# Performance work log

Measured on AMD Instinct MI355X. Metric: run time of the kernel, lower is better.

The kernel has to match this reference:

```python
import jax, jax.numpy as jnp
import numpy as np

BLOCK_SIZE = 256


def setup_inputs() -> dict:
    key = jax.random.key(0)
    k1, k2, k3, k4 = jax.random.split(key, 4)
    B, T, C, H = 512, 256, 384, 64
    x = jax.random.normal(k1, (B, T, C), dtype=jnp.float32)
    Wk = jax.random.normal(k2, (H, C), dtype=jnp.float32) * (1.0 / np.sqrt(C))
    Wq = jax.random.normal(k3, (H, C), dtype=jnp.float32) * (1.0 / np.sqrt(C))
    Wv = jax.random.normal(k4, (H, C), dtype=jnp.float32) * (1.0 / np.sqrt(C))
    return {"x": x, "Wk": Wk, "Wq": Wq, "Wv": Wv}


def reference(x, Wk, Wq, Wv):
    # x: [B, T, C]; Wk/Wq/Wv: [H, C] (torch nn.Linear weight layout, bias=False)
    B, T, C = x.shape
    H = Wk.shape[0]
    k = jnp.einsum('btc,hc->bth', x, Wk)
    q = jnp.einsum('btc,hc->bth', x, Wq)
    v = jnp.einsum('btc,hc->bth', x, Wv)
    scale = 1.0 / jnp.sqrt(jnp.float32(H))
    scores = jnp.einsum('bqh,bkh->bqk', q, k) * scale  # [B, T, T]
    causal = jnp.tril(jnp.ones((T, T), dtype=bool))
    scores = jnp.where(causal, scores, -jnp.inf)
    weights = jax.nn.softmax(scores, axis=-1)
    # dropout is identity in eval mode
    out = jnp.einsum('bqk,bkh->bqh', weights, v)  # [B, T, H]
    return out
```

## Files before the change

kernel.cpp:

```cpp
#include <hip/hip_runtime.h>
#include <hip/hip_bf16.h>
#include <math.h>

#define TT 256
#define CC 384
#define HH 64

typedef float v4f   __attribute__((ext_vector_type(4)));
typedef short short8 __attribute__((ext_vector_type(8)));

#define MFMA(a, b, c) __builtin_amdgcn_mfma_f32_16x16x32_bf16((a), (b), (c), 0, 0, 0)

__device__ __forceinline__ unsigned short f2bf(float f) {
    unsigned int u = __float_as_uint(f);
    u += 0x7FFFu + ((u >> 16) & 1u);
    return (unsigned short)(u >> 16);
}

__device__ __forceinline__ ushort4 f2bf4(float4 f) {
    union { __hip_bfloat162 h2[2]; ushort4 u4; } cv;
    cv.h2[0] = __float22bfloat162_rn(make_float2(f.x, f.y));
    cv.h2[1] = __float22bfloat162_rn(make_float2(f.z, f.w));
    return cv.u4;
}

#define KLOOP_BARRIER() do {                                   \
    asm volatile("s_waitcnt lgkmcnt(0)" ::: "memory");         \
    __builtin_amdgcn_s_barrier();                              \
    __builtin_amdgcn_sched_barrier(0);                         \
} while (0)

#define QSCALE 0.18033688f

__global__ __launch_bounds__(512, 4)
void qkv_proj(const float* __restrict__ x, const float* __restrict__ Wkp,
              const float* __restrict__ Wqp, const float* __restrict__ Wvp,
              unsigned short* __restrict__ qg, unsigned short* __restrict__ kg,
              unsigned short* __restrict__ vtg)
{
    __shared__ unsigned short sm[17408];
    unsigned short* x_s = sm;
    unsigned short* w_s = sm + 5120;
    unsigned short* epi = sm;

    const int tid  = threadIdx.x;
    const int wave = tid >> 6;
    const int lane = tid & 63;
    const int col  = lane & 15;
    const int quad = lane >> 4;
    const int row0 = blockIdx.x * 128;

    const int lr  = tid >> 3;
    const int lc4 = (tid & 7) * 4;

    const float* xp  = x   + (size_t)(row0 + lr) * CC + lc4;
    const float* wqp = Wqp + (size_t)lr * CC + lc4;
    const float* wkp = Wkp + (size_t)lr * CC + lc4;
    const float* wvp = Wvp + (size_t)lr * CC + lc4;

    v4f acc[12];
    #pragma unroll
    for (int j = 0; j < 12; ++j) acc[j] = (v4f){0.f, 0.f, 0.f, 0.f};

    float4 xA0 = *(const float4*)(xp);
    float4 xA1 = *(const float4*)(xp + 64 * CC);
    float4 wqA = *(const float4*)(wqp);
    float4 wkA = *(const float4*)(wkp);
    float4 wvA = *(const float4*)(wvp);

    const int afrag_off = (wave * 16 + col) * 40 + quad * 8;

    #pragma unroll
    for (int s = 0; s < 12; ++s) {
        float4 xB0, xB1, wqB, wkB, wvB;
        if (s < 11) {
            const int k0 = (s + 1) * 32;
            xB0 = *(const float4*)(xp + k0);
            xB1 = *(const float4*)(xp + 64 * CC + k0);
            wqB = *(const float4*)(wqp + k0);
            wkB = *(const float4*)(wkp + k0);
            wvB = *(const float4*)(wvp + k0);
        }
        KLOOP_BARRIER();
        *(ushort4*)&x_s[lr * 40 + lc4]         = f2bf4(xA0);
        *(ushort4*)&x_s[(lr + 64) * 40 + lc4]  = f2bf4(xA1);
        *(ushort4*)&w_s[lr * 40 + lc4]         = f2bf4(wqA);
        *(ushort4*)&w_s[(64 + lr) * 40 + lc4]  = f2bf4(wkA);
        *(ushort4*)&w_s[(128 + lr) * 40 + lc4] = f2bf4(wvA);
        KLOOP_BARRIER();
        const short8 a = *(const short8*)&x_s[afrag_off];
        #pragma unroll
        for (int nt = 0; nt < 12; ++nt) {
            const short8 bf = *(const short8*)&w_s[(nt * 16 + col) * 40 + quad * 8];
            acc[nt] = MFMA(a, bf, acc[nt]);
        }
        if (s < 11) { xA0 = xB0; xA1 = xB1; wqA = wqB; wkA = wkB; wvA = wvB; }
    }

    const int b    = row0 >> 8;
    const int half = (row0 >> 7) & 1;

    __syncthreads();
    #pragma unroll
    for (int nt = 0; nt < 8; ++nt) {
        #pragma unroll
        for (int r = 0; r < 4; ++r) {
            const int rl = wave * 16 + quad * 4 + r;
            const int n  = nt * 16 + col;
            float v = acc[nt][r];
            if (nt < 4) v *= QSCALE;
            epi[rl * 136 + n] = f2bf(v);
        }
    }
    __syncthreads();
    #pragma unroll
    for (int p = 0; p < 4; ++p) {
        const int idx = tid + p * 512;
        const int r = idx >> 4, ch = idx & 15;
        const short8 v = *(const short8*)&epi[r * 136 + ch * 8];
        const size_t base = (size_t)(row0 + r) * 64 + (ch & 7) * 8;
        if (ch < 8) *(short8*)&qg[base] = v;
        else        *(short8*)&kg[base] = v;
    }

    __syncthreads();
    #pragma unroll
    for (int nt = 8; nt < 12; ++nt) {
        #pragma unroll
        for (int r = 0; r < 4; ++r) {
            const int rl = wave * 16 + quad * 4 + r;
            const int h  = nt * 16 + col - 128;
            epi[h * 136 + rl] = f2bf(acc[nt][r]);
        }
    }
    __syncthreads();
    #pragma unroll
    for (int p = 0; p < 2; ++p) {
        const int idx = tid + p * 512;
        const int h = idx >> 4, ch = idx & 15;
        const short8 v = *(const short8*)&epi[h * 136 + ch * 8];
        *(short8*)&vtg[((size_t)b * 64 + h) * 256 + half * 128 + ch * 8] = v;
    }
}

__global__ __launch_bounds__(256, 4)
void attn(const unsigned short* __restrict__ qg, const unsigned short* __restrict__ kg,
          const unsigned short* __restrict__ vtg, float* __restrict__ out)
{
    __shared__ unsigned short Pb_all[4 * 16 * 40];
    const int tid  = threadIdx.x;
    const int wave = tid >> 6;
    const int lane = tid & 63;
    const int col  = lane & 15;
    const int quad = lane >> 4;
    const int b    = blockIdx.x >> 1;
    const int g    = blockIdx.x & 1;

    unsigned short* Pb = Pb_all + wave * 640;
    const unsigned short* kb_base = kg  + (size_t)b * 256 * 64;
    const unsigned short* vt_base = vtg + (size_t)b * 64 * 256;

    #pragma unroll
    for (int mi = 0; mi < 2; ++mi) {
        const int j  = g * 4 + wave;
        const int qt = mi ? (15 - j) : j;
        const size_t qoff = ((size_t)b * 256 + qt * 16 + col) * 64 + quad * 8;
        const short8 aq0 = *(const short8*)(qg + qoff);
        const short8 aq1 = *(const short8*)(qg + qoff + 32);

        float lsum[4];
        v4f oacc[4];
        #pragma unroll
        for (int r = 0; r < 4; ++r) lsum[r] = 0.f;
        #pragma unroll
        for (int hn = 0; hn < 4; ++hn) oacc[hn] = (v4f){0.f, 0.f, 0.f, 0.f};

        const int nch = qt / 2 + 1;
        short8 b00, b01, b10, b11;
        {
            const int ko0 = col * 64 + quad * 8;
            const int ko1 = (16 + col) * 64 + quad * 8;
            b00 = *(const short8*)(kb_base + ko0);
            b01 = *(const short8*)(kb_base + ko0 + 32);
            b10 = *(const short8*)(kb_base + ko1);
            b11 = *(const short8*)(kb_base + ko1 + 32);
        }
        for (int kc = 0; kc < nch; ++kc) {
            const int kb = kc * 32;
            v4f s0 = (v4f){0.f, 0.f, 0.f, 0.f};
            v4f s1 = (v4f){0.f, 0.f, 0.f, 0.f};
            s0 = MFMA(aq0, b00, s0);
            s0 = MFMA(aq1, b01, s0);
            s1 = MFMA(aq0, b10, s1);
            s1 = MFMA(aq1, b11, s1);
            if (kc + 1 < nch) {
                const int ko0 = (kb + 32 + col) * 64 + quad * 8;
                const int ko1 = (kb + 48 + col) * 64 + quad * 8;
                b00 = *(const short8*)(kb_base + ko0);
                b01 = *(const short8*)(kb_base + ko0 + 32);
                b10 = *(const short8*)(kb_base + ko1);
                b11 = *(const short8*)(kb_base + ko1 + 32);
            }
            const bool diag = (kc == qt / 2);
            #pragma unroll
            for (int r = 0; r < 4; ++r) {
                const int t = qt * 16 + quad * 4 + r;
                float v0 = s0[r];
                float v1 = s1[r];
                if (diag) {
                    if (kb + col > t)      v0 = -1e30f;
                    if (kb + 16 + col > t) v1 = -1e30f;
                }
                const float p0 = exp2f(v0);
                const float p1 = exp2f(v1);
                lsum[r] += p0 + p1;
                Pb[(quad * 4 + r) * 40 + col]      = f2bf(p0);
                Pb[(quad * 4 + r) * 40 + 16 + col] = f2bf(p1);
            }
            __threadfence_block();
            const short8 ap = *(const short8*)&Pb[col * 40 + quad * 8];
            #pragma unroll
            for (int hn = 0; hn < 4; ++hn) {
                const short8 bv = *(const short8*)(vt_base + (hn * 16 + col) * 256 + kb + quad * 8);
                oacc[hn] = MFMA(ap, bv, oacc[hn]);
            }
        }

        #pragma unroll
        for (int r = 0; r < 4; ++r) {
            float l = lsum[r];
            l += __shfl_xor(l, 1);
            l += __shfl_xor(l, 2);
            l += __shfl_xor(l, 4);
            l += __shfl_xor(l, 8);
            const int t = qt * 16 + quad * 4 + r;
            const float inv = 1.0f / l;
            float* op = out + ((size_t)b * TT + t) * HH;
            #pragma unroll
            for (int hn = 0; hn < 4; ++hn)
                op[hn * 16 + col] = oacc[hn][r] * inv;
        }
    }
}

extern "C" void kernel_launch(void* const* d_in, const int* in_sizes, int n_in,
                              void* d_out, int out_size, void* d_ws, size_t ws_size,
                              hipStream_t stream) {
    const float* x  = (const float*)d_in[0];
    const float* Wk = (const float*)d_in[1];
    const float* Wq = (const float*)d_in[2];
    const float* Wv = (const float*)d_in[3];
    float* out = (float*)d_out;

    unsigned short* qg  = (unsigned short*)d_ws;
    unsigned short* kg  = qg + (size_t)512 * 256 * 64;
    unsigned short* vtg = kg + (size_t)512 * 256 * 64;

    qkv_proj<<<dim3(1024), dim3(512), 0, stream>>>(x, Wk, Wq, Wv, qg, kg, vtg);
    attn<<<dim3(1024), dim3(256), 0, stream>>>(qg, kg, vtg, out);
}
```

Before: 334.6 us.

## Fuse QKV projection and causal attention into one kernel with LDS-resident Q/K/V

Replaces the two-kernel pipeline with a single kernel, one block per batch. The block projects all 256 rows of Q, K and V into LDS in MFMA-fragment-friendly layouts, then runs causal attention straight from LDS. This removes writing Q/K/V^T to a global workspace and reading them back, plus one kernel launch. In exchange it needs about 124KB of LDS per block, which limits residency to one block per CU and cuts the number of blocks in flight.

```diff
diff --git a/kernel.cpp b/kernel.cpp
--- a/kernel.cpp
+++ b/kernel.cpp
@@ -32,141 +32,112 @@
 
 #define QSCALE 0.18033688f
 
-__global__ __launch_bounds__(512, 4)
-void qkv_proj(const float* __restrict__ x, const float* __restrict__ Wkp,
-              const float* __restrict__ Wqp, const float* __restrict__ Wvp,
-              unsigned short* __restrict__ qg, unsigned short* __restrict__ kg,
-              unsigned short* __restrict__ vtg)
+#define XS_OFF 0
+#define WS_OFF 5120
+#define QF_OFF 12800
+#define KF_OFF 29184
+#define VF_OFF 45568
+#define SM_TOTAL 61952
+
+__global__ __launch_bounds__(512, 2)
+void fused_attn(const float* __restrict__ x, const float* __restrict__ Wkp,
+                const float* __restrict__ Wqp, const float* __restrict__ Wvp,
+                float* __restrict__ out)
 {
-    __shared__ unsigned short sm[17408];
-    unsigned short* x_s = sm;
-    unsigned short* w_s = sm + 5120;
-    unsigned short* epi = sm;
+    __shared__ unsigned short sm[SM_TOTAL];
+    unsigned short* x_s = sm + XS_OFF;
+    unsigned short* w_s = sm + WS_OFF;
 
     const int tid  = threadIdx.x;
     const int wave = tid >> 6;
     const int lane = tid & 63;
     const int col  = lane & 15;
     const int quad = lane >> 4;
-    const int row0 = blockIdx.x * 128;
+    const int b    = blockIdx.x;
 
     const int lr  = tid >> 3;
     const int lc4 = (tid & 7) * 4;
 
-    const float* xp  = x   + (size_t)(row0 + lr) * CC + lc4;
     const float* wqp = Wqp + (size_t)lr * CC + lc4;
     const float* wkp = Wkp + (size_t)lr * CC + lc4;
     const float* wvp = Wvp + (size_t)lr * CC + lc4;
 
-    v4f acc[12];
-    #pragma unroll
-    for (int j = 0; j < 12; ++j) acc[j] = (v4f){0.f, 0.f, 0.f, 0.f};
-
-    float4 xA0 = *(const float4*)(xp);
-    float4 xA1 = *(const float4*)(xp + 64 * CC);
-    float4 wqA = *(const float4*)(wqp);
-    float4 wkA = *(const float4*)(wkp);
-    float4 wvA = *(const float4*)(wvp);
-
     const int afrag_off = (wave * 16 + col) * 40 + quad * 8;
 
-    #pragma unroll
-    for (int s = 0; s < 12; ++s) {
-        float4 xB0, xB1, wqB, wkB, wvB;
-        if (s < 11) {
-            const int k0 = (s + 1) * 32;
-            xB0 = *(const float4*)(xp + k0);
-            xB1 = *(const float4*)(xp + 64 * CC + k0);
-            wqB = *(const float4*)(wqp + k0);
-            wkB = *(const float4*)(wkp + k0);
-            wvB = *(const float4*)(wvp + k0);
-        }
-        KLOOP_BARRIER();
-        *(ushort4*)&x_s[lr * 40 + lc4]         = f2bf4(xA0);
-        *(ushort4*)&x_s[(lr + 64) * 40 + lc4]  = f2bf4(xA1);
-        *(ushort4*)&w_s[lr * 40 + lc4]         = f2bf4(wqA);
-        *(ushort4*)&w_s[(64 + lr) * 40 + lc4]  = f2bf4(wkA);
-        *(ushort4*)&w_s[(128 + lr) * 40 + lc4] = f2bf4(wvA);
-        KLOOP_BARRIER();
-        const short8 a = *(const short8*)&x_s[afrag_off];
+    #pragma unroll 1
+    for (int half = 0; half < 2; ++half) {
+        const float* xp = x + ((size_t)b * 256 + half * 128 + lr) * CC + lc4;
+
+        v4f acc[12];
+        #pragma unroll
+        for (int j = 0; j < 12; ++j) acc[j] = (v4f){0.f, 0.f, 0.f, 0.f};
+
+        float4 xA0 = *(const float4*)(xp);
+        float4 xA1 = *(const float4*)(xp + 64 * CC);
+        float4 wqA = *(const float4*)(wqp);
+        float4 wkA = *(const float4*)(wkp);
+        float4 wvA = *(const float4*)(wvp);
+
+        #pragma unroll
+        for (int s = 0; s < 12; ++s) {
+            float4 xB0, xB1, wqB, wkB, wvB;
+            if (s < 11) {
+                const int k0 = (s + 1) * 32;
+                xB0 = *(const float4*)(xp + k0);
+                xB1 = *(const float4*)(xp + 64 * CC + k0);
+                wqB = *(const float4*)(wqp + k0);
+                wkB = *(const float4*)(wkp + k0);
+                wvB = *(const float4*)(wvp + k0);
+            }
+            KLOOP_BARRIER();
+            *(ushort4*)&x_s[lr * 40 + lc4]         = f2bf4(xA0);
+            *(ushort4*)&x_s[(lr + 64) * 40 + lc4]  = f2bf4(xA1);
+            *(ushort4*)&w_s[lr * 40 + lc4]         = f2bf4(wqA);
+            *(ushort4*)&w_s[(64 + lr) * 40 + lc4]  = f2bf4(wkA);
+            *(ushort4*)&w_s[(128 + lr) * 40 + lc4] = f2bf4(wvA);
+            KLOOP_BARRIER();
+            const short8 a = *(const short8*)&x_s[afrag_off];
+            #pragma unroll
+            for (int nt = 0; nt < 12; ++nt) {
+                const short8 bf = *(const short8*)&w_s[(nt * 16 + col) * 40 + quad * 8];
+                acc[nt] = MFMA(a, bf, acc[nt]);
+            }
+            if (s < 11) { xA0 = xB0; xA1 = xB1; wqA = wqB; wkA = wkB; wvA = wvB; }
+        }
+
         #pragma unroll
         for (int nt = 0; nt < 12; ++nt) {
-            const short8 bf = *(const short8*)&w_s[(nt * 16 + col) * 40 + quad * 8];
-            acc[nt] = MFMA(a, bf, acc[nt]);
-        }
-        if (s < 11) { xA0 = xB0; xA1 = xB1; wqA = wqB; wkA = wkB; wvA = wvB; }
-    }
-
-    const int b    = row0 >> 8;
-    const int half = (row0 >> 7) & 1;
-
-    __syncthreads();
-    #pragma unroll
-    for (int nt = 0; nt < 8; ++nt) {
-        #pragma unroll
-        for (int r = 0; r < 4; ++r) {
-            const int rl = wave * 16 + quad * 4 + r;
-            const int n  = nt * 16 + col;
-            float v = acc[nt][r];
-            if (nt < 4) v *= QSCALE;
-            epi[rl * 136 + n] = f2bf(v);
+            #pragma unroll
+            for (int r = 0; r < 4; ++r) {
+                const int rl   = wave * 16 + quad * 4 + r;
+                const int trow = half * 128 + rl;
+                const int n    = nt * 16 + col;
+                float v = acc[nt][r];
+                if (nt < 4) {
+                    const int h = n;
+                    sm[QF_OFF + (trow >> 4) * 1024 + (h >> 3) * 128
+                             + (trow & 15) * 8 + (h & 7)] = f2bf(v * QSCALE);
+                } else if (nt < 8) {
+                    const int h = n - 64;
+                    sm[KF_OFF + (trow >> 4) * 1024 + (h >> 3) * 128
+                             + (trow & 15) * 8 + (h & 7)] = f2bf(v);
+                } else {
+                    const int h = n - 128;
+                    sm[VF_OFF + (h >> 4) * 4096 + (trow >> 3) * 128
+                             + (h & 15) * 8 + (trow & 7)] = f2bf(v);
+                }
+            }
         }
     }
     __syncthreads();
-    #pragma unroll
-    for (int p = 0; p < 4; ++p) {
-        const int idx = tid + p * 512;
-        const int r = idx >> 4, ch = idx & 15;
-        const short8 v = *(const short8*)&epi[r * 136 + ch * 8];
-        const size_t base = (size_t)(row0 + r) * 64 + (ch & 7) * 8;
-        if (ch < 8) *(short8*)&qg[base] = v;
-        else        *(short8*)&kg[base] = v;
-    }
-
-    __syncthreads();
-    #pragma unroll
-    for (int nt = 8; nt < 12; ++nt) {
-        #pragma unroll
-        for (int r = 0; r < 4; ++r) {
-            const int rl = wave * 16 + quad * 4 + r;
-            const int h  = nt * 16 + col - 128;
-            epi[h * 136 + rl] = f2bf(acc[nt][r]);
-        }
-    }
-    __syncthreads();
-    #pragma unroll
-    for (int p = 0; p < 2; ++p) {
-        const int idx = tid + p * 512;
-        const int h = idx >> 4, ch = idx & 15;
-        const short8 v = *(const short8*)&epi[h * 136 + ch * 8];
-        *(short8*)&vtg[((size_t)b * 64 + h) * 256 + half * 128 + ch * 8] = v;
-    }
-}
-
-__global__ __launch_bounds__(256, 4)
-void attn(const unsigned short* __restrict__ qg, const unsigned short* __restrict__ kg,
-          const unsigned short* __restrict__ vtg, float* __restrict__ out)
-{
-    __shared__ unsigned short Pb_all[4 * 16 * 40];
-    const int tid  = threadIdx.x;
-    const int wave = tid >> 6;
-    const int lane = tid & 63;
-    const int col  = lane & 15;
-    const int quad = lane >> 4;
-    const int b    = blockIdx.x >> 1;
-    const int g    = blockIdx.x & 1;
-
-    unsigned short* Pb = Pb_all + wave * 640;
-    const unsigned short* kb_base = kg  + (size_t)b * 256 * 64;
-    const unsigned short* vt_base = vtg + (size_t)b * 64 * 256;
+
+    unsigned short* Pb = sm + wave * 640;
 
     #pragma unroll
     for (int mi = 0; mi < 2; ++mi) {
-        const int j  = g * 4 + wave;
-        const int qt = mi ? (15 - j) : j;
-        const size_t qoff = ((size_t)b * 256 + qt * 16 + col) * 64 + quad * 8;
-        const short8 aq0 = *(const short8*)(qg + qoff);
-        const short8 aq1 = *(const short8*)(qg + qoff + 32);
+        const int qt = mi ? (15 - wave) : wave;
+        const short8 aq0 = *(const short8*)&sm[QF_OFF + qt * 1024 + quad * 128 + col * 8];
+        const short8 aq1 = *(const short8*)&sm[QF_OFF + qt * 1024 + 512 + quad * 128 + col * 8];
 
         float lsum[4];
         v4f oacc[4];
@@ -178,12 +149,11 @@
         const int nch = qt / 2 + 1;
         short8 b00, b01, b10, b11;
         {
-            const int ko0 = col * 64 + quad * 8;
-            const int ko1 = (16 + col) * 64 + quad * 8;
-            b00 = *(const short8*)(kb_base + ko0);
-            b01 = *(const short8*)(kb_base + ko0 + 32);
-            b10 = *(const short8*)(kb_base + ko1);
-            b11 = *(const short8*)(kb_base + ko1 + 32);
+            const int t0 = KF_OFF + quad * 128 + col * 8;
+            b00 = *(const short8*)&sm[t0];
+            b01 = *(const short8*)&sm[t0 + 512];
+            b10 = *(const short8*)&sm[t0 + 1024];
+            b11 = *(const short8*)&sm[t0 + 1536];
         }
         for (int kc = 0; kc < nch; ++kc) {
             const int kb = kc * 32;
@@ -194,12 +164,11 @@
             s1 = MFMA(aq0, b10, s1);
             s1 = MFMA(aq1, b11, s1);
             if (kc + 1 < nch) {
-                const int ko0 = (kb + 32 + col) * 64 + quad * 8;
-                const int ko1 = (kb + 48 + col) * 64 + quad * 8;
-                b00 = *(const short8*)(kb_base + ko0);
-                b01 = *(const short8*)(kb_base + ko0 + 32);
-                b10 = *(const short8*)(kb_base + ko1);
-                b11 = *(const short8*)(kb_base + ko1 + 32);
+                const int t0 = KF_OFF + (kc + 1) * 2048 + quad * 128 + col * 8;
+                b00 = *(const short8*)&sm[t0];
+                b01 = *(const short8*)&sm[t0 + 512];
+                b10 = *(const short8*)&sm[t0 + 1024];
+                b11 = *(const short8*)&sm[t0 + 1536];
             }
             const bool diag = (kc == qt / 2);
             #pragma unroll
@@ -221,7 +190,8 @@
             const short8 ap = *(const short8*)&Pb[col * 40 + quad * 8];
             #pragma unroll
             for (int hn = 0; hn < 4; ++hn) {
-                const short8 bv = *(const short8*)(vt_base + (hn * 16 + col) * 256 + kb + quad * 8);
+                const short8 bv = *(const short8*)&sm[VF_OFF + hn * 4096
+                                        + (kc * 4 + quad) * 128 + col * 8];
                 oacc[hn] = MFMA(ap, bv, oacc[hn]);
             }
         }
@@ -251,11 +221,7 @@
     const float* Wq = (const float*)d_in[2];
     const float* Wv = (const float*)d_in[3];
     float* out = (float*)d_out;
-
-    unsigned short* qg  = (unsigned short*)d_ws;
-    unsigned short* kg  = qg + (size_t)512 * 256 * 64;
-    unsigned short* vtg = kg + (size_t)512 * 256 * 64;
-
-    qkv_proj<<<dim3(1024), dim3(512), 0, stream>>>(x, Wk, Wq, Wv, qg, kg, vtg);
-    attn<<<dim3(1024), dim3(256), 0, stream>>>(qg, kg, vtg, out);
-}
+    (void)d_ws; (void)ws_size;
+
+    fused_attn<<<dim3(512), dim3(512), 0, stream>>>(x, Wk, Wq, Wv, out);
+}
```

Result: faster. 308.9 us (-7.7%).
